# Performance work log

Measured on AMD Instinct MI355X. Metric: run time of the kernel, lower is better.

The kernel has to match this reference:

```python
import jax, jax.numpy as jnp
import numpy as np

EMBED = 512
WINDOW = 64

def setup_inputs() -> dict:
    key = jax.random.key(0)
    ks = jax.random.split(key, 5)
    B, S, E = 4, 4096, EMBED
    s = 1.0 / np.sqrt(E)
    x = jax.random.normal(ks[0], (B, S, E), dtype=jnp.float32)
    W_qkv = jax.random.uniform(ks[1], (E, 3 * E), minval=-s, maxval=s, dtype=jnp.float32)
    b_qkv = jax.random.uniform(ks[2], (3 * E,), minval=-s, maxval=s, dtype=jnp.float32)
    W_out = jax.random.uniform(ks[3], (E, E), minval=-s, maxval=s, dtype=jnp.float32)
    b_out = jax.random.uniform(ks[4], (E,), minval=-s, maxval=s, dtype=jnp.float32)
    return {"x": x, "W_qkv": W_qkv, "b_qkv": b_qkv, "W_out": W_out, "b_out": b_out}

def reference(x, W_qkv, b_qkv, W_out, b_out):
    B, S, E = x.shape
    scale = jnp.sqrt(jnp.asarray(E, dtype=x.dtype))
    qkv = x @ W_qkv + b_qkv                    # [B,S,3E]
    q, k, v = jnp.split(qkv, 3, axis=-1)       # each [B,S,E]
    scores = jnp.einsum('bqe,bke->bqk', q, k) / scale  # [B,S,S]
    pos = jnp.arange(S)
    dist = pos[None, :] - pos[:, None]         # [S,S]
    window_mask = jnp.abs(dist) <= WINDOW
    neg_inf = jnp.asarray(-jnp.inf, dtype=scores.dtype)
    scores = jnp.where(window_mask[None, :, :], scores, neg_inf)
    attn = jax.nn.softmax(scores, axis=-1)     # every row has in-window entries
    attended = jnp.einsum('bqk,bke->bqe', attn, v)
    return attended @ W_out + b_out
```

## Files before the change

kernel.cpp:

```cpp
#include <hip/hip_runtime.h>

typedef __attribute__((ext_vector_type(8))) _Float16 f16x8;
typedef __attribute__((ext_vector_type(4))) _Float16 f16x4;
typedef __attribute__((ext_vector_type(4))) float f32x4;
typedef __attribute__((address_space(1))) const char gc_char;
typedef __attribute__((address_space(3))) char ls_char;

#define MFMA(a, b, c) __builtin_amdgcn_mfma_f32_16x16x32_f16((a), (b), (c), 0, 0, 0)
#define FENCE() asm volatile("" ::: "memory")
#define BARRIER() do { FENCE(); __builtin_amdgcn_s_barrier(); FENCE(); } while (0)
#define VMW(n) asm volatile("s_waitcnt vmcnt(" #n ")" ::: "memory")

static constexpr int SEQ = 4096;
static constexpr int EMB = 512;
static constexpr float QSCALE = 0.04419417382415922f;

__device__ __forceinline__ void gl_lds16(const void* g, void* l) {
    __builtin_amdgcn_global_load_lds((gc_char*)g, (ls_char*)l, 16, 0, 0);
}

__global__ void k_prep(const float* __restrict__ x, _Float16* __restrict__ xb,
                       const float* __restrict__ Wq, _Float16* __restrict__ WqT,
                       const float* __restrict__ Wo, _Float16* __restrict__ WoT) {
    const int bid = blockIdx.x, tid = threadIdx.x;
    if (bid < 4096) {
        long i = (long)bid * 256 + tid;
        const float4* p = (const float4*)x + i * 2;
        float4 a = p[0], b = p[1];
        f16x8 v;
        v[0] = (_Float16)a.x; v[1] = (_Float16)a.y; v[2] = (_Float16)a.z; v[3] = (_Float16)a.w;
        v[4] = (_Float16)b.x; v[5] = (_Float16)b.y; v[6] = (_Float16)b.z; v[7] = (_Float16)b.w;
        *(f16x8*)(xb + i * 8) = v;
    } else {
        __shared__ float Ls[64][65];
        int t = bid - 4096;
        const float* W; _Float16* WT; int N, k0, n0;
        if (t < 192) { W = Wq; WT = WqT; N = 1536; k0 = (t & 7) * 64; n0 = (t >> 3) * 64; }
        else { t -= 192; W = Wo; WT = WoT; N = 512; k0 = (t & 7) * 64; n0 = (t >> 3) * 64; }
        int c = tid & 63, r4 = tid >> 6;
#pragma unroll
        for (int i = 0; i < 16; ++i) {
            int row = i * 4 + r4;
            Ls[row][c] = W[(long)(k0 + row) * N + n0 + c];
        }
        __syncthreads();
#pragma unroll
        for (int i = 0; i < 16; ++i) {
            int row = i * 4 + r4;
            WT[(long)(n0 + row) * 512 + k0 + c] = (_Float16)Ls[c][row];
        }
    }
}

__launch_bounds__(512, 1) __global__
void k_gemm_qkv(const _Float16* __restrict__ A, const _Float16* __restrict__ BT,
                const float* __restrict__ bias,
                _Float16* __restrict__ Qo, _Float16* __restrict__ Ko, _Float16* __restrict__ VT) {
    extern __shared__ __align__(16) char smem[];
    const int tid = threadIdx.x, lane = tid & 63, w = tid >> 6, g = lane >> 4, f = lane & 15;
    const int wrow = w >> 2, wcol = w & 3;
    const int bid = blockIdx.x;
    const int swz = (bid & 7) * 96 + (bid >> 3);
    const int brow = swz / 6, bcol = swz - brow * 6;
    const long row0 = (long)brow * 128;
    const int col0 = bcol * 256;
    const char* Abase = (const char*)A + row0 * 1024;
    const char* Bbase = (const char*)BT + (long)col0 * 1024;

    f32x4 acc[4][4] = {};
    f16x8 a[2][2], breg[2][2][2];

    auto stageA = [&](int h, char* dst, int kt) {
        int rr = tid >> 3;
        int ch = (tid & 7) ^ (rr & 7);
        int grow = h * 32 + (rr & 31) + (rr >> 5) * 64;
        gl_lds16(Abase + (long)grow * 1024 + kt * 128 + ch * 16, dst + h * 8192 + tid * 16);
    };
    auto stageB = [&](int h, char* dst, int kt) {
#pragma unroll
        for (int it = 0; it < 2; ++it) {
            int s = it * 512 + tid;
            int cc = s >> 3;
            int ch = (s & 7) ^ (cc & 7);
            int gcol = h * 32 + (cc & 31) + (cc >> 5) * 64;
            gl_lds16(Bbase + (long)gcol * 1024 + kt * 128 + ch * 16,
                     dst + 16384 + h * 16384 + s * 16);
        }
    };
    auto ldA = [&](const char* buf, int mh) {
#pragma unroll
        for (int mi = 0; mi < 2; ++mi)
#pragma unroll
            for (int ks = 0; ks < 2; ++ks) {
                int rr = wrow * 32 + mi * 16 + f;
                int cl = ks * 4 + g;
                a[mi][ks] = *(const f16x8*)(buf + mh * 8192 + rr * 128 + ((cl ^ (rr & 7)) << 4));
            }
    };
    auto ldB = [&](const char* buf, int nh) {
#pragma unroll
        for (int ni = 0; ni < 2; ++ni)
#pragma unroll
            for (int ks = 0; ks < 2; ++ks) {
                int cc = wcol * 32 + ni * 16 + f;
                int cl = ks * 4 + g;
                breg[nh][ni][ks] =
                    *(const f16x8*)(buf + 16384 + nh * 16384 + cc * 128 + ((cl ^ (cc & 7)) << 4));
            }
    };
    auto mfma8 = [&](int mh, int nh) {
        __builtin_amdgcn_s_setprio(1);
#pragma unroll
        for (int mi = 0; mi < 2; ++mi)
#pragma unroll
            for (int ni = 0; ni < 2; ++ni)
#pragma unroll
                for (int ks = 0; ks < 2; ++ks)
                    acc[mh * 2 + mi][nh * 2 + ni] =
                        MFMA(a[mi][ks], breg[nh][ni][ks], acc[mh * 2 + mi][nh * 2 + ni]);
        __builtin_amdgcn_s_setprio(0);
    };

    stageB(0, smem, 0);
    stageA(0, smem, 0); stageA(1, smem, 0);
    stageB(1, smem, 0);
    VMW(3);
    BARRIER();

    for (int kt = 0; kt < 8; ++kt) {
        const char* cur = smem + (kt & 1) * 49152;
        char* nxt = smem + ((kt + 1) & 1) * 49152;
        const bool last = (kt == 7);
        ldA(cur, 0); ldB(cur, 0);
        if (!last) stageB(0, nxt, kt + 1);
        BARRIER();
        mfma8(0, 0);
        if (!last) { VMW(2); } else { VMW(0); }
        BARRIER();
        ldB(cur, 1);
        if (!last) { stageA(0, nxt, kt + 1); stageA(1, nxt, kt + 1); }
        BARRIER();
        mfma8(0, 1);
        BARRIER();
        ldA(cur, 1);
        if (!last) stageB(1, nxt, kt + 1);
        BARRIER();
        mfma8(1, 0);
        BARRIER();
        mfma8(1, 1);
        if (!last) { VMW(3); }
        BARRIER();
    }

    float bv[4];
#pragma unroll
    for (int ni = 0; ni < 4; ++ni) bv[ni] = bias[col0 + wcol * 64 + ni * 16 + f];

    if (col0 >= 1024) {
#pragma unroll
        for (int mi = 0; mi < 4; ++mi)
#pragma unroll
            for (int ni = 0; ni < 4; ++ni) {
                int r0 = wrow * 64 + mi * 16 + g * 4;
                int c = wcol * 64 + ni * 16 + f;
                f16x4 v4;
#pragma unroll
                for (int j = 0; j < 4; ++j) v4[j] = (_Float16)(acc[mi][ni][j] + bv[ni]);
                *(f16x4*)(smem + c * 256 + ((r0 * 2) ^ ((c & 7) << 4))) = v4;
            }
        __syncthreads();
        int bb = (int)(row0 >> 12);
        _Float16* vt = VT + ((long)bb * 512 + (col0 - 1024)) * 4096 + (row0 & 4095);
#pragma unroll
        for (int it = 0; it < 8; ++it) {
            int slot = it * 512 + tid;
            int e = slot >> 4, ch = slot & 15;
            f16x8 v = *(const f16x8*)(smem + e * 256 + ((ch * 16) ^ ((e & 7) << 4)));
            *(f16x8*)(vt + (long)e * 4096 + ch * 8) = v;
        }
    } else {
        const float sc = (col0 < 512) ? QSCALE : 1.0f;
#pragma unroll
        for (int mi = 0; mi < 4; ++mi)
#pragma unroll
            for (int ni = 0; ni < 4; ++ni)
#pragma unroll
                for (int j = 0; j < 4; ++j) {
                    int r = wrow * 64 + mi * 16 + g * 4 + j;
                    int c = wcol * 64 + ni * 16 + f;
                    float v = (acc[mi][ni][j] + bv[ni]) * sc;
                    int pc = ((c >> 3) + ((r >> 2) & 7) * 2) & 31;
                    *(_Float16*)(smem + r * 512 + pc * 16 + (c & 7) * 2) = (_Float16)v;
                }
        __syncthreads();
        _Float16* dst = (col0 < 512) ? Qo : Ko;
        int cofs = (col0 < 512) ? col0 : col0 - 512;
#pragma unroll
        for (int it = 0; it < 8; ++it) {
            int slot = it * 512 + tid;
            int r = slot >> 5, ch = slot & 31;
            int pc = (ch + ((r >> 2) & 7) * 2) & 31;
            f16x8 v = *(const f16x8*)(smem + r * 512 + pc * 16);
            *(f16x8*)(dst + (row0 + r) * 512 + cofs + ch * 8) = v;
        }
    }
}

__launch_bounds__(512, 4) __global__
void k_attn(const _Float16* __restrict__ Qb, const _Float16* __restrict__ Kb,
            const _Float16* __restrict__ VT, const _Float16* __restrict__ WoT,
            const float* __restrict__ bout, float* __restrict__ Out) {
    extern __shared__ __align__(16) char smem[];
    char* buf = smem;
    char* Pl = smem + 49152;
    float* Mp = (float*)(smem + 59904);
    float* Lp = (float*)(smem + 60416);
    char* att = smem;
    char* wbf = smem + 32768;

    const int tid = threadIdx.x, w = tid >> 6, lane = tid & 63, g = lane >> 4, f = lane & 15;
    const int rh = w >> 2, kh = w & 3;
    const int NT = (kh < 2) ? 3 : 2;
    const int bid = blockIdx.x;
    const int swzb = (bid & 7) * 64 + (bid >> 3);
    const int b = swzb >> 7, qt = swzb & 127;
    const int q0 = qt * 32, kbase = q0 - 64;
    const long bofs = (long)b * SEQ;

    const _Float16* qr = Qb + (bofs + q0 + rh * 16 + f) * EMB;
    f16x8 qf[16];
#pragma unroll
    for (int s = 0; s < 16; ++s) qf[s] = *(const f16x8*)(qr + s * 32 + g * 8);

    auto stageK = [&](int ec) {
#pragma unroll
        for (int it = 0; it < 5; ++it) {
            int slot = it * 512 + tid;
            int r = slot >> 4, c = slot & 15;
            int cs = c ^ (r & 7);
            int key = min(max(kbase + r, 0), SEQ - 1);
            gl_lds16(Kb + (bofs + key) * EMB + ec * 128 + cs * 8, buf + slot * 16);
        }
    };
    auto stageVT = [&](int ec) {
#pragma unroll
        for (int it = 0; it < 6; ++it) {
            int slot = it * 512 + tid;
            int r = slot / 24, c = slot - r * 24;
            int cs = c ^ (r & 7);
            int k0 = min(max(kbase + cs * 8, 0), SEQ - 8);
            gl_lds16(VT + ((long)b * 512 + ec * 128 + r) * 4096 + k0, buf + slot * 16);
        }
    };

    f32x4 sacc[3] = {};
    stageK(0);
    __syncthreads();
#pragma unroll
    for (int ec = 0; ec < 4; ++ec) {
#pragma unroll
        for (int kk = 0; kk < 4; ++kk) {
#pragma unroll
            for (int t = 0; t < 3; ++t) {
                if (t < NT) {
                    int n = (kh + t * 4) * 16 + f;
                    f16x8 bf = *(const f16x8*)(buf + n * 256 + (((kk * 4 + g) ^ (n & 7)) << 4));
                    sacc[t] = MFMA(qf[ec * 4 + kk], bf, sacc[t]);
                }
            }
        }
        __syncthreads();
        if (ec < 3) { stageK(ec + 1); __syncthreads(); }
    }

    float m[4] = {-3e30f, -3e30f, -3e30f, -3e30f}, l[4] = {0.f, 0.f, 0.f, 0.f};
#pragma unroll
    for (int t = 0; t < 3; ++t) {
        if (t < NT) {
            int key = kbase + (kh + t * 4) * 16 + f;
            bool kv = (key >= 0) && (key < SEQ);
#pragma unroll
            for (int j = 0; j < 4; ++j) {
                int d = key - (q0 + rh * 16 + g * 4 + j);
                bool valid = kv && (d >= -64) && (d <= 64);
                float s = valid ? sacc[t][j] : -3e30f;
                sacc[t][j] = s;
                m[j] = fmaxf(m[j], s);
            }
        }
    }
#pragma unroll
    for (int j = 0; j < 4; ++j) {
        m[j] = fmaxf(m[j], __shfl_xor(m[j], 1));
        m[j] = fmaxf(m[j], __shfl_xor(m[j], 2));
        m[j] = fmaxf(m[j], __shfl_xor(m[j], 4));
        m[j] = fmaxf(m[j], __shfl_xor(m[j], 8));
    }
    if (f == 0) {
#pragma unroll
        for (int j = 0; j < 4; ++j) Mp[kh * 32 + rh * 16 + g * 4 + j] = m[j];
    }
    __syncthreads();
#pragma unroll
    for (int j = 0; j < 4; ++j) {
        int r = rh * 16 + g * 4 + j;
        m[j] = fmaxf(fmaxf(Mp[r], Mp[32 + r]), fmaxf(Mp[64 + r], Mp[96 + r]));
    }
#pragma unroll
    for (int t = 0; t < 3; ++t) {
        if (t < NT) {
#pragma unroll
            for (int j = 0; j < 4; ++j) {
                float p = __expf(sacc[t][j] - m[j]);
                sacc[t][j] = p;
                l[j] += p;
            }
        }
    }
#pragma unroll
    for (int j = 0; j < 4; ++j) {
        l[j] += __shfl_xor(l[j], 1);
        l[j] += __shfl_xor(l[j], 2);
        l[j] += __shfl_xor(l[j], 4);
        l[j] += __shfl_xor(l[j], 8);
    }
    if (f == 0) {
#pragma unroll
        for (int j = 0; j < 4; ++j) Lp[kh * 32 + rh * 16 + g * 4 + j] = l[j];
    }
#pragma unroll
    for (int t = 0; t < 3; ++t) {
        if (t < NT) {
#pragma unroll
            for (int j = 0; j < 4; ++j)
                *(_Float16*)(Pl + (rh * 16 + g * 4 + j) * 336 +
                             ((kh + t * 4) * 16 + f) * 2) = (_Float16)sacc[t][j];
        }
    }
    __syncthreads();
    stageVT(0);

    float rl[4];
#pragma unroll
    for (int j = 0; j < 4; ++j) {
        int r = rh * 16 + g * 4 + j;
        rl[j] = 1.0f / (Lp[r] + Lp[32 + r] + Lp[64 + r] + Lp[96 + r]);
    }
    f16x8 pf[5];
#pragma unroll
    for (int kc = 0; kc < 5; ++kc)
        pf[kc] = *(const f16x8*)(Pl + (rh * 16 + f) * 336 + kc * 64 + g * 16);
    __syncthreads();

    f32x4 oacc[4][2] = {};
#pragma unroll
    for (int ec = 0; ec < 4; ++ec) {
#pragma unroll
        for (int kc = 0; kc < 5; ++kc) {
#pragma unroll
            for (int nt = 0; nt < 2; ++nt) {
                int e = kh * 32 + nt * 16 + f;
                f16x8 vf = *(const f16x8*)(buf + e * 384 + (((kc * 4 + g) ^ (e & 7)) << 4));
                oacc[ec][nt] = MFMA(pf[kc], vf, oacc[ec][nt]);
            }
        }
        __syncthreads();
        if (ec < 3) { stageVT(ec + 1); __syncthreads(); }
    }

    auto stageW = [&](int u) {
#pragma unroll
        for (int i = 0; i < 4; ++i) {
            int s = i * 512 + tid;
            int col = s >> 2, ch = s & 3;
            gl_lds16(WoT + (long)col * 512 + u * 32 + ((ch ^ (col & 3)) * 8), wbf + s * 16);
        }
    };
#pragma unroll
    for (int ec = 0; ec < 4; ++ec)
#pragma unroll
        for (int nt = 0; nt < 2; ++nt)
#pragma unroll
            for (int j = 0; j < 4; ++j) {
                int row = rh * 16 + g * 4 + j;
                int col = ec * 128 + kh * 32 + nt * 16 + f;
                *(_Float16*)(att + row * 1024 + ((col * 2) ^ ((row & 7) << 4))) =
                    (_Float16)(oacc[ec][nt][j] * rl[j]);
            }
    stageW(0);
    __syncthreads();

    float bv2[8];
#pragma unroll
    for (int nt = 0; nt < 8; ++nt) bv2[nt] = bout[kh * 128 + nt * 16 + f];

    f32x4 acc2[8] = {};
    for (int u = 0; u < 16; ++u) {
        int arow = rh * 16 + f;
        f16x8 a2 = *(const f16x8*)(att + arow * 1024 + ((u * 64 + g * 16) ^ ((arow & 7) << 4)));
        __builtin_amdgcn_s_setprio(1);
#pragma unroll
        for (int nt = 0; nt < 8; ++nt) {
            int col = kh * 128 + nt * 16 + f;
            f16x8 b2 = *(const f16x8*)(wbf + col * 64 + ((g * 16) ^ ((col & 3) << 4)));
            acc2[nt] = MFMA(a2, b2, acc2[nt]);
        }
        __builtin_amdgcn_s_setprio(0);
        __syncthreads();
        if (u < 15) { stageW(u + 1); __syncthreads(); }
    }

#pragma unroll
    for (int nt = 0; nt < 8; ++nt) {
        long r0 = bofs + q0 + rh * 16 + g * 4;
        int c = kh * 128 + nt * 16 + f;
#pragma unroll
        for (int j = 0; j < 4; ++j)
            Out[(r0 + j) * 512 + c] = acc2[nt][j] + bv2[nt];
    }
}

extern "C" void kernel_launch(void* const* d_in, const int* in_sizes, int n_in,
                              void* d_out, int out_size, void* d_ws, size_t ws_size,
                              hipStream_t stream) {
    const float* x     = (const float*)d_in[0];
    const float* W_qkv = (const float*)d_in[1];
    const float* b_qkv = (const float*)d_in[2];
    const float* W_out = (const float*)d_in[3];
    const float* b_out = (const float*)d_in[4];

    char* ws = (char*)d_ws;
    _Float16* xb    = (_Float16*)(ws);
    _Float16* WqkvT = (_Float16*)(ws + 16777216);
    _Float16* WoutT = (_Float16*)(ws + 16777216 + 1572864);
    _Float16* Qb    = (_Float16*)(ws + 18874368);
    _Float16* Kb    = (_Float16*)(ws + 18874368 + 16777216);
    _Float16* VT    = (_Float16*)(ws + 18874368 + 33554432);
    float* out = (float*)d_out;

    (void)hipFuncSetAttribute((const void*)k_gemm_qkv,
                              hipFuncAttributeMaxDynamicSharedMemorySize, 98304);
    (void)hipFuncSetAttribute((const void*)k_attn,
                              hipFuncAttributeMaxDynamicSharedMemorySize, 65536);

    k_prep<<<4352, 256, 0, stream>>>(x, xb, W_qkv, WqkvT, W_out, WoutT);
    k_gemm_qkv<<<768, 512, 98304, stream>>>(xb, WqkvT, b_qkv, Qb, Kb, VT);
    k_attn<<<512, 512, 65536, stream>>>(Qb, Kb, VT, WoutT, b_out, out);
}
```

Baseline: 86.66 us.

## Split output projection into separate GEMM kernel and double-buffer attention staging

The attention kernel now stages K and V^T in smaller 64-wide chunks across two LDS buffers, prefetching the next chunk while computing the current one. This removes the extra barrier per stage. The fused output projection, which reloaded W_out per 32-row tile, moves into a dedicated 128x256-tile pipelined GEMM kernel reading an fp16 attended buffer that reuses the xb workspace. This adds an extra launch and a global round trip of the attended activations, in exchange for better W_out reuse and lower LDS use in the attention kernel.

```diff
diff --git a/kernel.cpp b/kernel.cpp
--- a/kernel.cpp
+++ b/kernel.cpp
@@ -208,15 +208,12 @@
 
 __launch_bounds__(512, 4) __global__
 void k_attn(const _Float16* __restrict__ Qb, const _Float16* __restrict__ Kb,
-            const _Float16* __restrict__ VT, const _Float16* __restrict__ WoT,
-            const float* __restrict__ bout, float* __restrict__ Out) {
+            const _Float16* __restrict__ VT, _Float16* __restrict__ Att) {
     extern __shared__ __align__(16) char smem[];
-    char* buf = smem;
+    char* buf[2] = { smem, smem + 24576 };
     char* Pl = smem + 49152;
     float* Mp = (float*)(smem + 59904);
     float* Lp = (float*)(smem + 60416);
-    char* att = smem;
-    char* wbf = smem + 32768;
 
     const int tid = threadIdx.x, w = tid >> 6, lane = tid & 63, g = lane >> 4, f = lane & 15;
     const int rh = w >> 2, kh = w & 3;
@@ -232,45 +229,48 @@
 #pragma unroll
     for (int s = 0; s < 16; ++s) qf[s] = *(const f16x8*)(qr + s * 32 + g * 8);
 
-    auto stageK = [&](int ec) {
-#pragma unroll
-        for (int it = 0; it < 5; ++it) {
+    auto stageK = [&](int ec, char* dst) {
+#pragma unroll
+        for (int it = 0; it < 3; ++it) {
             int slot = it * 512 + tid;
-            int r = slot >> 4, c = slot & 15;
-            int cs = c ^ (r & 7);
-            int key = min(max(kbase + r, 0), SEQ - 1);
-            gl_lds16(Kb + (bofs + key) * EMB + ec * 128 + cs * 8, buf + slot * 16);
-        }
-    };
-    auto stageVT = [&](int ec) {
-#pragma unroll
-        for (int it = 0; it < 6; ++it) {
+            if (slot < 1280) {
+                int r = slot >> 3, c = slot & 7;
+                int cs = c ^ (r & 7);
+                int key = min(max(kbase + r, 0), SEQ - 1);
+                gl_lds16(Kb + (bofs + key) * EMB + ec * 64 + cs * 8, dst + slot * 16);
+            }
+        }
+    };
+    auto stageVT = [&](int ec, char* dst) {
+#pragma unroll
+        for (int it = 0; it < 3; ++it) {
             int slot = it * 512 + tid;
             int r = slot / 24, c = slot - r * 24;
             int cs = c ^ (r & 7);
             int k0 = min(max(kbase + cs * 8, 0), SEQ - 8);
-            gl_lds16(VT + ((long)b * 512 + ec * 128 + r) * 4096 + k0, buf + slot * 16);
+            gl_lds16(VT + ((long)b * 512 + ec * 64 + r) * 4096 + k0, dst + slot * 16);
         }
     };
 
     f32x4 sacc[3] = {};
-    stageK(0);
+    stageK(0, buf[0]);
     __syncthreads();
-#pragma unroll
-    for (int ec = 0; ec < 4; ++ec) {
-#pragma unroll
-        for (int kk = 0; kk < 4; ++kk) {
+    for (int ec = 0; ec < 8; ++ec) {
+        if (ec < 7) stageK(ec + 1, buf[(ec + 1) & 1]);
+        else stageVT(0, buf[0]);
+        const char* kb = buf[ec & 1];
+#pragma unroll
+        for (int kk = 0; kk < 2; ++kk) {
 #pragma unroll
             for (int t = 0; t < 3; ++t) {
                 if (t < NT) {
                     int n = (kh + t * 4) * 16 + f;
-                    f16x8 bf = *(const f16x8*)(buf + n * 256 + (((kk * 4 + g) ^ (n & 7)) << 4));
-                    sacc[t] = MFMA(qf[ec * 4 + kk], bf, sacc[t]);
+                    f16x8 bf = *(const f16x8*)(kb + n * 128 + (((kk * 4 + g) ^ (n & 7)) << 4));
+                    sacc[t] = MFMA(qf[ec * 2 + kk], bf, sacc[t]);
                 }
             }
         }
         __syncthreads();
-        if (ec < 3) { stageK(ec + 1); __syncthreads(); }
     }
 
     float m[4] = {-3e30f, -3e30f, -3e30f, -3e30f}, l[4] = {0.f, 0.f, 0.f, 0.f};
@@ -338,7 +338,6 @@
         }
     }
     __syncthreads();
-    stageVT(0);
 
     float rl[4];
 #pragma unroll
@@ -350,74 +349,135 @@
 #pragma unroll
     for (int kc = 0; kc < 5; ++kc)
         pf[kc] = *(const f16x8*)(Pl + (rh * 16 + f) * 336 + kc * 64 + g * 16);
-    __syncthreads();
-
-    f32x4 oacc[4][2] = {};
-#pragma unroll
-    for (int ec = 0; ec < 4; ++ec) {
+
+    _Float16* ob = Att + (bofs + q0 + rh * 16 + g * 4) * EMB + kh * 16 + f;
+    for (int vc = 0; vc < 8; ++vc) {
+        if (vc < 7) stageVT(vc + 1, buf[(vc + 1) & 1]);
+        const char* vb = buf[vc & 1];
+        int e = kh * 16 + f;
+        f32x4 o = {};
 #pragma unroll
         for (int kc = 0; kc < 5; ++kc) {
-#pragma unroll
-            for (int nt = 0; nt < 2; ++nt) {
-                int e = kh * 32 + nt * 16 + f;
-                f16x8 vf = *(const f16x8*)(buf + e * 384 + (((kc * 4 + g) ^ (e & 7)) << 4));
-                oacc[ec][nt] = MFMA(pf[kc], vf, oacc[ec][nt]);
-            }
-        }
+            f16x8 vf = *(const f16x8*)(vb + e * 384 + (((kc * 4 + g) ^ (e & 7)) << 4));
+            o = MFMA(pf[kc], vf, o);
+        }
+#pragma unroll
+        for (int j = 0; j < 4; ++j)
+            ob[(long)j * EMB + vc * 64] = (_Float16)(o[j] * rl[j]);
         __syncthreads();
-        if (ec < 3) { stageVT(ec + 1); __syncthreads(); }
-    }
-
-    auto stageW = [&](int u) {
-#pragma unroll
-        for (int i = 0; i < 4; ++i) {
-            int s = i * 512 + tid;
-            int col = s >> 2, ch = s & 3;
-            gl_lds16(WoT + (long)col * 512 + u * 32 + ((ch ^ (col & 3)) * 8), wbf + s * 16);
-        }
-    };
-#pragma unroll
-    for (int ec = 0; ec < 4; ++ec)
-#pragma unroll
-        for (int nt = 0; nt < 2; ++nt)
-#pragma unroll
-            for (int j = 0; j < 4; ++j) {
-                int row = rh * 16 + g * 4 + j;
-                int col = ec * 128 + kh * 32 + nt * 16 + f;
-                *(_Float16*)(att + row * 1024 + ((col * 2) ^ ((row & 7) << 4))) =
-                    (_Float16)(oacc[ec][nt][j] * rl[j]);
-            }
-    stageW(0);
-    __syncthreads();
-
-    float bv2[8];
-#pragma unroll
-    for (int nt = 0; nt < 8; ++nt) bv2[nt] = bout[kh * 128 + nt * 16 + f];
-
-    f32x4 acc2[8] = {};
-    for (int u = 0; u < 16; ++u) {
-        int arow = rh * 16 + f;
-        f16x8 a2 = *(const f16x8*)(att + arow * 1024 + ((u * 64 + g * 16) ^ ((arow & 7) << 4)));
+    }
+}
+
+__launch_bounds__(512, 1) __global__
+void k_gemm_out(const _Float16* __restrict__ A, const _Float16* __restrict__ BT,
+                const float* __restrict__ bias, float* __restrict__ out) {
+    extern __shared__ __align__(16) char smem[];
+    const int tid = threadIdx.x, lane = tid & 63, w = tid >> 6, g = lane >> 4, f = lane & 15;
+    const int wrow = w >> 2, wcol = w & 3;
+    const int bid = blockIdx.x;
+    const int swz = (bid & 7) * 32 + (bid >> 3);
+    const int brow = swz >> 1, bcol = swz & 1;
+    const long row0 = (long)brow * 128;
+    const int col0 = bcol * 256;
+    const char* Abase = (const char*)A + row0 * 1024;
+    const char* Bbase = (const char*)BT + (long)col0 * 1024;
+
+    f32x4 acc[4][4] = {};
+    f16x8 a[2][2], breg[2][2][2];
+
+    auto stageA = [&](int h, char* dst, int kt) {
+        int rr = tid >> 3;
+        int ch = (tid & 7) ^ (rr & 7);
+        int grow = h * 32 + (rr & 31) + (rr >> 5) * 64;
+        gl_lds16(Abase + (long)grow * 1024 + kt * 128 + ch * 16, dst + h * 8192 + tid * 16);
+    };
+    auto stageB = [&](int h, char* dst, int kt) {
+#pragma unroll
+        for (int it = 0; it < 2; ++it) {
+            int s = it * 512 + tid;
+            int cc = s >> 3;
+            int ch = (s & 7) ^ (cc & 7);
+            int gcol = h * 32 + (cc & 31) + (cc >> 5) * 64;
+            gl_lds16(Bbase + (long)gcol * 1024 + kt * 128 + ch * 16,
+                     dst + 16384 + h * 16384 + s * 16);
+        }
+    };
+    auto ldA = [&](const char* buf, int mh) {
+#pragma unroll
+        for (int mi = 0; mi < 2; ++mi)
+#pragma unroll
+            for (int ks = 0; ks < 2; ++ks) {
+                int rr = wrow * 32 + mi * 16 + f;
+                int cl = ks * 4 + g;
+                a[mi][ks] = *(const f16x8*)(buf + mh * 8192 + rr * 128 + ((cl ^ (rr & 7)) << 4));
+            }
+    };
+    auto ldB = [&](const char* buf, int nh) {
+#pragma unroll
+        for (int ni = 0; ni < 2; ++ni)
+#pragma unroll
+            for (int ks = 0; ks < 2; ++ks) {
+                int cc = wcol * 32 + ni * 16 + f;
+                int cl = ks * 4 + g;
+                breg[nh][ni][ks] =
+                    *(const f16x8*)(buf + 16384 + nh * 16384 + cc * 128 + ((cl ^ (cc & 7)) << 4));
+            }
+    };
+    auto mfma8 = [&](int mh, int nh) {
         __builtin_amdgcn_s_setprio(1);
 #pragma unroll
-        for (int nt = 0; nt < 8; ++nt) {
-            int col = kh * 128 + nt * 16 + f;
-            f16x8 b2 = *(const f16x8*)(wbf + col * 64 + ((g * 16) ^ ((col & 3) << 4)));
-            acc2[nt] = MFMA(a2, b2, acc2[nt]);
-        }
+        for (int mi = 0; mi < 2; ++mi)
+#pragma unroll
+            for (int ni = 0; ni < 2; ++ni)
+#pragma unroll
+                for (int ks = 0; ks < 2; ++ks)
+                    acc[mh * 2 + mi][nh * 2 + ni] =
+                        MFMA(a[mi][ks], breg[nh][ni][ks], acc[mh * 2 + mi][nh * 2 + ni]);
         __builtin_amdgcn_s_setprio(0);
-        __syncthreads();
-        if (u < 15) { stageW(u + 1); __syncthreads(); }
-    }
-
-#pragma unroll
-    for (int nt = 0; nt < 8; ++nt) {
-        long r0 = bofs + q0 + rh * 16 + g * 4;
-        int c = kh * 128 + nt * 16 + f;
-#pragma unroll
-        for (int j = 0; j < 4; ++j)
-            Out[(r0 + j) * 512 + c] = acc2[nt][j] + bv2[nt];
-    }
+    };
+
+    stageB(0, smem, 0);
+    stageA(0, smem, 0); stageA(1, smem, 0);
+    stageB(1, smem, 0);
+    VMW(3);
+    BARRIER();
+
+    for (int kt = 0; kt < 8; ++kt) {
+        const char* cur = smem + (kt & 1) * 49152;
+        char* nxt = smem + ((kt + 1) & 1) * 49152;
+        const bool last = (kt == 7);
+        ldA(cur, 0); ldB(cur, 0);
+        if (!last) stageB(0, nxt, kt + 1);
+        BARRIER();
+        mfma8(0, 0);
+        if (!last) { VMW(2); } else { VMW(0); }
+        BARRIER();
+        ldB(cur, 1);
+        if (!last) { stageA(0, nxt, kt + 1); stageA(1, nxt, kt + 1); }
+        BARRIER();
+        mfma8(0, 1);
+        BARRIER();
+        ldA(cur, 1);
+        if (!last) stageB(1, nxt, kt + 1);
+        BARRIER();
+        mfma8(1, 0);
+        BARRIER();
+        mfma8(1, 1);
+        if (!last) { VMW(3); }
+        BARRIER();
+    }
+
+#pragma unroll
+    for (int mi = 0; mi < 4; ++mi)
+#pragma unroll
+        for (int ni = 0; ni < 4; ++ni) {
+            long r0 = row0 + wrow * 64 + mi * 16 + g * 4;
+            int c = col0 + wcol * 64 + ni * 16 + f;
+            float bv = bias[c];
+#pragma unroll
+            for (int j = 0; j < 4; ++j)
+                out[(r0 + j) * 512 + c] = acc[mi][ni][j] + bv;
+        }
 }
 
 extern "C" void kernel_launch(void* const* d_in, const int* in_sizes, int n_in,
@@ -436,14 +496,18 @@
     _Float16* Qb    = (_Float16*)(ws + 18874368);
     _Float16* Kb    = (_Float16*)(ws + 18874368 + 16777216);
     _Float16* VT    = (_Float16*)(ws + 18874368 + 33554432);
+    _Float16* Att   = xb;
     float* out = (float*)d_out;
 
     (void)hipFuncSetAttribute((const void*)k_gemm_qkv,
                               hipFuncAttributeMaxDynamicSharedMemorySize, 98304);
     (void)hipFuncSetAttribute((const void*)k_attn,
-                              hipFuncAttributeMaxDynamicSharedMemorySize, 65536);
+                              hipFuncAttributeMaxDynamicSharedMemorySize, 60928);
+    (void)hipFuncSetAttribute((const void*)k_gemm_out,
+                              hipFuncAttributeMaxDynamicSharedMemorySize, 98304);
 
     k_prep<<<4352, 256, 0, stream>>>(x, xb, W_qkv, WqkvT, W_out, WoutT);
     k_gemm_qkv<<<768, 512, 98304, stream>>>(xb, WqkvT, b_qkv, Qb, Kb, VT);
-    k_attn<<<512, 512, 65536, stream>>>(Qb, Kb, VT, WoutT, b_out, out);
+    k_attn<<<512, 512, 60928, stream>>>(Qb, Kb, VT, Att);
+    k_gemm_out<<<256, 512, 98304, stream>>>(Att, WoutT, b_out, out);
 }
```

New measurement: 82.40 us. 1.05x faster.
